# Optimization experiments

Hardware: AMD Instinct MI355X
Metric: run time of the kernel (lower is better)

The kernel has to match this reference:

```python
import jax, jax.numpy as jnp
import numpy as np

B, S, F_IN, D, H, L, E, DFF, OUT = 16, 512, 46, 256, 8, 6, 8, 1024, 3


def _ln(x, s, b, eps=1e-5):
    m = x.mean(-1, keepdims=True)
    v = ((x - m) ** 2).mean(-1, keepdims=True)
    return (x - m) / jnp.sqrt(v + eps) * s + b


def _mha(q_in, kv_in, qkv_w, qkv_b, out_w, out_b, h):
    # torch nn.MultiheadAttention (batch_first), eval mode (no dropout)
    d = q_in.shape[-1]
    dh = d // h
    wq, wk, wv = jnp.split(qkv_w, 3, axis=0)
    bq, bk, bv = jnp.split(qkv_b, 3)
    q = (q_in @ wq.T + bq).reshape(q_in.shape[0], q_in.shape[1], h, dh)
    k = (kv_in @ wk.T + bk).reshape(kv_in.shape[0], kv_in.shape[1], h, dh)
    v = (kv_in @ wv.T + bv).reshape(kv_in.shape[0], kv_in.shape[1], h, dh)
    attn = jax.nn.softmax(jnp.einsum('bqhd,bkhd->bhqk', q, k) / jnp.sqrt(jnp.float32(dh)), axis=-1)
    o = jnp.einsum('bhqk,bkhd->bqhd', attn, v).reshape(q_in.shape[0], q_in.shape[1], d)
    return o @ out_w.T + out_b


def _moe(x, gate_w, gate_b, e_w1, e_b1, e_w2, e_b2, top_k=2):
    # Faithful to source: EVERY expert runs its dense FFN over all tokens,
    # then outputs are mixed by the top-k gate weights (zero for unrouted experts).
    logits = x @ gate_w.T + gate_b                      # (B,S,E)
    tk_logits, tk_idx = jax.lax.top_k(logits, top_k)    # (B,S,K)
    tk_probs = jax.nn.softmax(tk_logits, axis=-1)
    onehot = jax.nn.one_hot(tk_idx, logits.shape[-1], dtype=x.dtype)  # (B,S,K,E)
    weights = (onehot * tk_probs[..., None]).sum(-2)    # (B,S,E)
    hid = jax.nn.gelu(jnp.einsum('bsd,efd->bsef', x, e_w1) + e_b1, approximate=False)  # (B,S,E,DFF)
    out_e = jnp.einsum('bsef,edf->bsed', hid, e_w2) + e_b2                             # (B,S,E,D)
    out = jnp.einsum('bsed,bse->bsd', out_e, weights)
    probs = jax.nn.softmax(logits, axis=-1)
    aux = logits.shape[-1] * jnp.sum(probs.mean(axis=(0, 1)) ** 2)
    return out, aux


def _posenc(s, d):
    pos = jnp.arange(s, dtype=jnp.float32)[:, None]
    div = jnp.exp(jnp.arange(0, d, 2, dtype=jnp.float32) * (-np.log(10000.0) / d))
    pe = jnp.zeros((s, d), jnp.float32)
    pe = pe.at[:, 0::2].set(jnp.sin(pos * div)).at[:, 1::2].set(jnp.cos(pos * div))
    return pe


def _forward(x, in_w, in_b, l_qkv_w, l_qkv_b, l_out_w, l_out_b, gate_w, gate_b,
             e_w1, e_b1, e_w2, e_b2, ln1_s, ln1_b, ln2_s, ln2_b,
             p_qkv_w, p_qkv_b, p_out_w, p_out_b,
             a_w1, a_b1, a_ln1s, a_ln1b, a_w2, a_b2, a_ln2s, a_ln2b, a_w3, a_b3,
             pr_w1, pr_b1, pr_ln1s, pr_ln1b, pr_w2, pr_b2, pr_ln2s, pr_ln2b, pr_w3, pr_b3):
    h = x @ in_w.T + in_b + _posenc(x.shape[1], D)[None]
    aux_total = jnp.float32(0.0)
    # NB: source builds ModuleList([encoder_layer]*L) with the SAME instance -> shared weights
    for _ in range(L):
        attn = _mha(h, h, l_qkv_w, l_qkv_b, l_out_w, l_out_b, H)
        h = _ln(h + attn, ln1_s, ln1_b)
        moe_out, aux = _moe(h, gate_w, gate_b, e_w1, e_b1, e_w2, e_b2)
        aux_total = aux_total + aux
        h = _ln(h + moe_out, ln2_s, ln2_b)
    pooled = _mha(h[:, -1:, :], h, p_qkv_w, p_qkv_b, p_out_w, p_out_b, H)[:, 0]  # (B,D)
    # action head: Linear -> GELU -> LN -> Linear -> GELU -> LN -> Linear
    a = jax.nn.gelu(pooled @ a_w1.T + a_b1, approximate=False)
    a = _ln(a, a_ln1s, a_ln1b)
    a = jax.nn.gelu(a @ a_w2.T + a_b2, approximate=False)
    a = _ln(a, a_ln2s, a_ln2b)
    action = a @ a_w3.T + a_b3
    # profit head: Linear -> LN -> GELU -> Linear -> LN -> GELU -> Linear
    p = jax.nn.gelu(_ln(pooled @ pr_w1.T + pr_b1, pr_ln1s, pr_ln1b), approximate=False)
    p = jax.nn.gelu(_ln(p @ pr_w2.T + pr_b2, pr_ln2s, pr_ln2b), approximate=False)
    profit = p @ pr_w3.T + pr_b3
    return action, profit, aux_total


def setup_inputs() -> dict:
    key = jax.random.key(0)
    ks = iter(jax.random.split(key, 64))
    def w(shape, scale=0.02):
        return jax.random.normal(next(ks), shape, jnp.float32) * scale
    d2, d4 = D // 2, D // 4
    return dict(
        x=jax.random.normal(next(ks), (B, S, F_IN), jnp.float32),
        in_w=w((D, F_IN)), in_b=jnp.zeros(D),
        l_qkv_w=w((3 * D, D)), l_qkv_b=jnp.zeros(3 * D), l_out_w=w((D, D)), l_out_b=jnp.zeros(D),
        gate_w=w((E, D)), gate_b=jnp.zeros(E),
        e_w1=w((E, DFF, D)), e_b1=jnp.zeros((E, DFF)), e_w2=w((E, D, DFF)), e_b2=jnp.zeros((E, D)),
        ln1_s=jnp.ones(D), ln1_b=jnp.zeros(D), ln2_s=jnp.ones(D), ln2_b=jnp.zeros(D),
        p_qkv_w=w((3 * D, D)), p_qkv_b=jnp.zeros(3 * D), p_out_w=w((D, D)), p_out_b=jnp.zeros(D),
        a_w1=w((d2, D)), a_b1=jnp.zeros(d2), a_ln1s=jnp.ones(d2), a_ln1b=jnp.zeros(d2),
        a_w2=w((d4, d2)), a_b2=jnp.zeros(d4), a_ln2s=jnp.ones(d4), a_ln2b=jnp.zeros(d4),
        a_w3=w((OUT, d4)), a_b3=jnp.zeros(OUT),
        pr_w1=w((D, D)), pr_b1=jnp.zeros(D), pr_ln1s=jnp.ones(D), pr_ln1b=jnp.zeros(D),
        pr_w2=w((d2, D)), pr_b2=jnp.zeros(d2), pr_ln2s=jnp.ones(d2), pr_ln2b=jnp.zeros(d2),
        pr_w3=w((1, d2)), pr_b3=jnp.zeros(1),
    )


def reference(x, in_w, in_b, l_qkv_w, l_qkv_b, l_out_w, l_out_b, gate_w, gate_b,
              e_w1, e_b1, e_w2, e_b2, ln1_s, ln1_b, ln2_s, ln2_b,
              p_qkv_w, p_qkv_b, p_out_w, p_out_b,
              a_w1, a_b1, a_ln1s, a_ln1b, a_w2, a_b2, a_ln2s, a_ln2b, a_w3, a_b3,
              pr_w1, pr_b1, pr_ln1s, pr_ln1b, pr_w2, pr_b2, pr_ln2s, pr_ln2b, pr_w3, pr_b3):
    return _forward(x, in_w, in_b, l_qkv_w, l_qkv_b, l_out_w, l_out_b, gate_w, gate_b,
                    e_w1, e_b1, e_w2, e_b2, ln1_s, ln1_b, ln2_s, ln2_b,
                    p_qkv_w, p_qkv_b, p_out_w, p_out_b,
                    a_w1, a_b1, a_ln1s, a_ln1b, a_w2, a_b2, a_ln2s, a_ln2b, a_w3, a_b3,
                    pr_w1, pr_b1, pr_ln1s, pr_ln1b, pr_w2, pr_b2, pr_ln2s, pr_ln2b, pr_w3, pr_b3)
```

## Files before the change

### kernel.cpp

```cpp
#include <hip/hip_runtime.h>
#include <hip/hip_bf16.h>
#include <math.h>


typedef __bf16 bf16;
typedef __bf16 bf16x8 __attribute__((ext_vector_type(8)));
typedef __bf16 bf16x4 __attribute__((ext_vector_type(4)));
typedef float f32x4 __attribute__((ext_vector_type(4)));

#define NIN 41

#define GLOAD_LDS(g, l)                                                    \
    __builtin_amdgcn_global_load_lds(                                      \
        (const __attribute__((address_space(1))) void*)(g),                \
        (__attribute__((address_space(3))) void*)(l), 16, 0, 0)

struct InTab {
    const void* src[NIN];
    unsigned off[NIN];
    unsigned n[NIN];
};

__device__ __forceinline__ float gelu_exact(float x) {
    return 0.5f * x * (1.0f + erff(x * 0.70710678118654752f));
// ... 125 lines not shown
            }
#pragma unroll
            for (int mt = 0; mt < MT; mt++)
#pragma unroll
                for (int nt = 0; nt < NT; nt++)
                    acc[mt][nt] = __builtin_amdgcn_mfma_f32_16x16x32_bf16(
                        af[mt], bfr[nt], acc[mt][nt], 0, 0, 0);
        }
        __syncthreads();
    }

    if (VTOUT && bn0g >= 512) {
#pragma unroll
        for (int mt = 0; mt < MT; mt++)
#pragma unroll
            for (int nt = 0; nt < NT; nt++) {
                const int gn = bn0g + wn0 + nt * 16 + frow;
                const float bv = (float)bias[gn];
                bf16x4 o4;
#pragma unroll
                for (int r = 0; r < 4; r++) o4[r] = (bf16)(acc[mt][nt][r] + bv);
                const int gm0 = bm0 + wm0 + mt * 16 + fquad * 4;
                const int d = gn - 512;
                *(bf16x4*)&vT[((size_t)((gm0 >> 9) * 8 + (d >> 5)) * 32 + (d & 31)) * 512 +
                              (gm0 & 511)] = o4;
            }
    } else {
        bf16* Cs = smem;
#pragma unroll
        for (int mt = 0; mt < MT; mt++)
#pragma unroll
            for (int nt = 0; nt < NT; nt++) {
                const int cl = wn0 + nt * 16 + frow;
                const float bv = (float)bias[bn0g + cl];
#pragma unroll
                for (int r = 0; r < 4; r++)
                    Cs[(wm0 + mt * 16 + fquad * 4 + r) * BN + cl] =
                        (bf16)(acc[mt][nt][r] + bv);
            }
        __syncthreads();
        constexpr int CPR = BN / 8;
        constexpr int CH = (BM * BN) / (256 * 8);
#pragma unroll
        for (int i = 0; i < CH; i++) {
            const int ch = tid + i * 256;
            const int row = ch / CPR;
            const int col = (ch % CPR) * 8;
            *(bf16x8*)&C[(size_t)(bm0 + row) * N + bn0g + col] =
                *(const bf16x8*)&Cs[row * BN + col];
        }
    }
}

__global__ __launch_bounds__(256) void gemm_moe_w1(
    const bf16* __restrict__ A, const bf16* __restrict__ Wb,
    const bf16* __restrict__ biasb, bf16* __restrict__ hid0,
    bf16* __restrict__ hid1, const int* __restrict__ list,
    const int* __restrict__ tile_ex, const int* __restrict__ ntiles) {
    constexpr int BM = 64, BN = 128, BK = 64;
    constexpr int N = 1024, K = 256;
    const int slot = (blockIdx.x >= 144) ? 1 : 0;
    const int xi = (int)blockIdx.x - slot * 144;
    if (xi >= (ntiles[slot] << 1)) return;
    __shared__ alignas(16) bf16 smem[BM * BK + BN * BK];
    bf16* As = smem;
    bf16* Ws = smem + BM * BK;
    const int* mylist = list + slot * 9216;
    const int e = tile_ex[slot * 72 + (xi >> 1)];
    const bf16* W = Wb + (size_t)e * N * K;
    const bf16* bias = biasb + e * N;
    bf16* C = slot ? hid1 : hid0;
    const int bm0 = xi * BM, bn0 = blockIdx.y * BN;
    const int tid = threadIdx.x;
    const int wave = tid >> 6, lane = tid & 63;
    const int wm0 = (wave >> 1) * 32, wn0 = (wave & 1) * 64;
    constexpr int MT = 2, NT = 4;
    f32x4 acc[MT][NT] = {};
    const int frow = lane & 15, fquad = lane >> 4;

    const bf16* ag[2];
    const bf16* bg[4];
    unsigned al[2], bl[4];
#pragma unroll
    for (int i = 0; i < 2; i++) {
        const int d = wave * 128 + i * 64 + lane;
        const int r = d >> 3, c = ((d & 7) ^ (r & 7)) * 8;
        ag[i] = A + (size_t)mylist[bm0 + r] * K + c;
        al[i] = (unsigned)(wave * 128 + i * 64) * 8u;
    }
#pragma unroll
    for (int i = 0; i < 4; i++) {
        const int d = wave * 256 + i * 64 + lane;
        const int r = d >> 3, c = ((d & 7) ^ (r & 7)) * 8;
        bg[i] = W + (size_t)(bn0 + r) * K + c;
        bl[i] = (unsigned)(wave * 256 + i * 64) * 8u;
    }

    for (int k0 = 0; k0 < K; k0 += BK) {
#pragma unroll
        for (int i = 0; i < 2; i++) GLOAD_LDS(ag[i] + k0, &As[al[i]]);
#pragma unroll
        for (int i = 0; i < 4; i++) GLOAD_LDS(bg[i] + k0, &Ws[bl[i]]);
        __syncthreads();
#pragma unroll
        for (int ks = 0; ks < 2; ks++) {
            bf16x8 af[MT], bfr[NT];
#pragma unroll
            for (int mt = 0; mt < MT; mt++) {
                const int r = wm0 + mt * 16 + frow;
                af[mt] = *(const bf16x8*)&As[SWZ(r, ks * 4 + fquad)];
            }
#pragma unroll
            for (int nt = 0; nt < NT; nt++) {
                const int r = wn0 + nt * 16 + frow;
                bfr[nt] = *(const bf16x8*)&Ws[SWZ(r, ks * 4 + fquad)];
            }
#pragma unroll
            for (int mt = 0; mt < MT; mt++)
#pragma unroll
                for (int nt = 0; nt < NT; nt++)
                    acc[mt][nt] = __builtin_amdgcn_mfma_f32_16x16x32_bf16(
                        af[mt], bfr[nt], acc[mt][nt], 0, 0, 0);
        }
        __syncthreads();
    }

    {
        bf16* Cs = smem;
#pragma unroll
        for (int mt = 0; mt < MT; mt++)
#pragma unroll
            for (int nt = 0; nt < NT; nt++) {
                const int cl = wn0 + nt * 16 + frow;
                const float bv = (float)bias[bn0 + cl];
#pragma unroll
                for (int r = 0; r < 4; r++)
                    Cs[(wm0 + mt * 16 + fquad * 4 + r) * BN + cl] =
                        (bf16)gelu_fast(acc[mt][nt][r] + bv);
            }
        __syncthreads();
#pragma unroll
        for (int i = 0; i < 4; i++) {
            const int ch = tid + i * 256;
            const int row = ch >> 4;
            const int col = (ch & 15) * 8;
            *(bf16x8*)&C[(size_t)(bm0 + row) * N + bn0 + col] =
                *(const bf16x8*)&Cs[row * BN + col];
        }
    }
}

__global__ __launch_bounds__(256) void gemm_moe_w2(
    const bf16* __restrict__ hid0, const bf16* __restrict__ hid1,
    const bf16* __restrict__ Wb, const bf16* __restrict__ biasb,
    bf16* __restrict__ moe0, bf16* __restrict__ moe1,
    const int* __restrict__ list, const float* __restrict__ lw,
    const int* __restrict__ tile_ex, const int* __restrict__ ntiles) {
    constexpr int BM = 64, BN = 64, BK = 64;
    constexpr int N = 256, K = 1024;
    const int slot = (blockIdx.x >= 144) ? 1 : 0;
    const int xi = (int)blockIdx.x - slot * 144;
    if (xi >= (ntiles[slot] << 1)) return;
    __shared__ alignas(16) bf16 smem[BM * BK + BN * BK];
    bf16* As = smem;
    bf16* Ws = smem + BM * BK;
    const bf16* A = slot ? hid1 : hid0;
    bf16* C = slot ? moe1 : moe0;
    const int* mylist = list + slot * 9216;
    const float* mylw = lw + slot * 9216;
    const int e = tile_ex[slot * 72 + (xi >> 1)];
    const bf16* W = Wb + (size_t)e * N * K;
    const bf16* bias = biasb + e * N;
    const int bm0 = xi * BM, bn0 = blockIdx.y * BN;
    const int tid = threadIdx.x;
    const int wave = tid >> 6, lane = tid & 63;
    const int wm0 = wave * 16;
    constexpr int NT = 4;
    f32x4 acc[NT] = {};
    const int frow = lane & 15, fquad = lane >> 4;

    const bf16* ag[2];
    const bf16* bg[2];
    unsigned al[2], bl[2];
#pragma unroll
    for (int i = 0; i < 2; i++) {
        const int d = wave * 128 + i * 64 + lane;
        const int r = d >> 3, c = ((d & 7) ^ (r & 7)) * 8;
        ag[i] = A + (size_t)(bm0 + r) * K + c;
        al[i] = (unsigned)(wave * 128 + i * 64) * 8u;
        bg[i] = W + (size_t)(bn0 + r) * K + c;
        bl[i] = al[i];
    }

    for (int k0 = 0; k0 < K; k0 += BK) {
#pragma unroll
        for (int i = 0; i < 2; i++) GLOAD_LDS(ag[i] + k0, &As[al[i]]);
#pragma unroll
        for (int i = 0; i < 2; i++) GLOAD_LDS(bg[i] + k0, &Ws[bl[i]]);
        __syncthreads();
#pragma unroll
        for (int ks = 0; ks < 2; ks++) {
            bf16x8 af, bfr[NT];
            af = *(const bf16x8*)&As[SWZ(wm0 + frow, ks * 4 + fquad)];
#pragma unroll
            for (int nt = 0; nt < NT; nt++) {
                const int r = nt * 16 + frow;
                bfr[nt] = *(const bf16x8*)&Ws[SWZ(r, ks * 4 + fquad)];
            }
#pragma unroll
            for (int nt = 0; nt < NT; nt++)
                acc[nt] = __builtin_amdgcn_mfma_f32_16x16x32_bf16(
                    af, bfr[nt], acc[nt], 0, 0, 0);
        }
        __syncthreads();
    }

    {
        bf16* Cs = smem;
        float lwv[4];
#pragma unroll
        for (int r = 0; r < 4; r++)
            lwv[r] = mylw[bm0 + wm0 + fquad * 4 + r];
#pragma unroll
        for (int nt = 0; nt < NT; nt++) {
            const int cl = nt * 16 + frow;
            const float bv = (float)bias[bn0 + cl];
#pragma unroll
            for (int r = 0; r < 4; r++)
                Cs[(wm0 + fquad * 4 + r) * BN + cl] =
                    (bf16)(lwv[r] * (acc[nt][r] + bv));
        }
        __syncthreads();
#pragma unroll
        for (int i = 0; i < 2; i++) {
            const int ch = tid + i * 256;
            const int row = ch >> 3;
            const int col = (ch & 7) * 8;
            *(bf16x8*)&C[(size_t)mylist[bm0 + row] * 256 + bn0 + col] =
                *(const bf16x8*)&Cs[row * BN + col];
        }
    }
}

__global__ __launch_bounds__(256) void input_proj_kernel(
    const bf16* __restrict__ x, const bf16* __restrict__ w,
    const bf16* __restrict__ b, bf16* __restrict__ h) {
    const int m = blockIdx.x, t = threadIdx.x;
    __shared__ float xs[46];
    if (t < 46) xs[t] = (float)x[m * 46 + t];
    __syncthreads();
    float acc = (float)b[t];
#pragma unroll
    for (int k = 0; k < 46; k++) acc += xs[k] * (float)w[t * 46 + k];
    const int s = m & 511;
    const int i = t >> 1;
    const float dv = expf((float)(2 * i) * (-9.210340371976184f / 256.0f));
    const float ang = (float)s * dv;
    const float pe = (t & 1) ? cosf(ang) : sinf(ang);
    h[(size_t)m * 256 + t] = (bf16)(acc + pe);
}

__global__ __launch_bounds__(256) void ln_kernel(
    bf16* __restrict__ h, const bf16* __restrict__ a0,
    const bf16* __restrict__ a1, const bf16* __restrict__ s,
    const bf16* __restrict__ b) {
    const int wv = threadIdx.x >> 6, lane = threadIdx.x & 63;
    const int m = blockIdx.x * 8 + wv * 2 + (lane >> 5);
    const int c0 = (lane & 31) * 8;
    const size_t off = (size_t)m * 256 + c0;
    bf16x8 hv = *(const bf16x8*)&h[off];
    bf16x8 av = *(const bf16x8*)&a0[off];
    bf16x8 bv2 = *(const bf16x8*)&a1[off];
    float x[8];
    float s1 = 0.0f, s2 = 0.0f;
#pragma unroll
    for (int j = 0; j < 8; j++) {
        x[j] = (float)hv[j] + (float)av[j] + (float)bv2[j];
        s1 += x[j];
        s2 += x[j] * x[j];
    }
#pragma unroll
    for (int msk = 1; msk < 32; msk <<= 1) {
        s1 += __shfl_xor(s1, msk, 64);
        s2 += __shfl_xor(s2, msk, 64);
    }
    const float mean = s1 * (1.0f / 256.0f);
    const float var = fmaxf(s2 * (1.0f / 256.0f) - mean * mean, 0.0f);
    const float inv = rsqrtf(var + 1e-5f);
    bf16x8 sv = *(const bf16x8*)&s[c0];
    bf16x8 bv = *(const bf16x8*)&b[c0];
    bf16x8 o;
#pragma unroll
    for (int j = 0; j < 8; j++)
        o[j] = (bf16)((x[j] - mean) * inv * (float)sv[j] + (float)bv[j]);
    *(bf16x8*)&h[off] = o;
}

__global__ __launch_bounds__(256) void proj_gate_ln_kernel(
    const bf16* __restrict__ A, const bf16* __restrict__ W,
    const bf16* __restrict__ bias, bf16* __restrict__ h,
    const bf16* __restrict__ lns, const bf16* __restrict__ lnb,
    const bf16* __restrict__ gw, const bf16* __restrict__ gb,
    int* __restrict__ top_e, float* __restrict__ top_w,
    int* __restrict__ g_hist, float* __restrict__ aux_sums) {
    __shared__ alignas(16) bf16 As[16 * 64];
    __shared__ alignas(16) bf16 Ws[256 * 64];
    __shared__ alignas(16) bf16 hs[16 * 264];
    __shared__ alignas(16) bf16 gws[8 * 264];
    __shared__ float rws1[4][16], rws2[4][16];
    __shared__ float meanv[16], invv[16];
    __shared__ float lg[128];
    __shared__ int sh_hist[16];
    __shared__ float sh_aux[8];

    const int bm0 = blockIdx.x * 16;
    const int tid = threadIdx.x;
    const int wave = tid >> 6, lane = tid & 63;
    const int wn0 = wave * 64;
    const int frow = lane & 15, fquad = lane >> 4;
    f32x4 acc[4] = {};

    const int da = (wave & 1) * 64 + lane;
    const int ra = da >> 3, ca = ((da & 7) ^ (ra & 7)) * 8;
    const bf16* ag = A + (size_t)(bm0 + ra) * 256 + ca;
    const unsigned al = (unsigned)((wave & 1) * 64) * 8u;
    const bf16* bg[8];
    unsigned bl[8];
#pragma unroll
    for (int i = 0; i < 8; i++) {
        const int d = wave * 512 + i * 64 + lane;
        const int r = d >> 3, c = ((d & 7) ^ (r & 7)) * 8;
        bg[i] = W + (size_t)r * 256 + c;
        bl[i] = (unsigned)(wave * 512 + i * 64) * 8u;
    }

    {
        const int rr = tid >> 4, ccb = (tid & 15) * 16;
        const bf16* src = &h[(size_t)(bm0 + rr) * 256 + ccb];
        bf16x8 v0 = *(const bf16x8*)&src[0];
        bf16x8 v1 = *(const bf16x8*)&src[8];
        bf16* dst = &hs[rr * 264 + ccb];
        *(bf16x8*)&dst[0] = v0;
        *(bf16x8*)&dst[8] = v1;
    }
    {
        const int e = tid >> 5, k = (tid & 31) * 8;
        *(bf16x8*)&gws[e * 264 + k] = *(const bf16x8*)&gw[e * 256 + k];
    }
    if (tid < 16) sh_hist[tid] = 0;
    if (tid < 8) sh_aux[tid] = 0.0f;

    for (int k0 = 0; k0 < 256; k0 += 64) {
        if (wave < 2) GLOAD_LDS(ag + k0, &As[al]);
#pragma unroll
        for (int i = 0; i < 8; i++) GLOAD_LDS(bg[i] + k0, &Ws[bl[i]]);
        __syncthreads();
#pragma unroll
        for (int ks = 0; ks < 2; ks++) {
            bf16x8 af, bfr[4];
            af = *(const bf16x8*)&As[SWZ(frow, ks * 4 + fquad)];
#pragma unroll
            for (int nt = 0; nt < 4; nt++)
                bfr[nt] = *(const bf16x8*)&Ws[SWZ(wn0 + nt * 16 + frow, ks * 4 + fquad)];
#pragma unroll
            for (int nt = 0; nt < 4; nt++)
                acc[nt] = __builtin_amdgcn_mfma_f32_16x16x32_bf16(
                    af, bfr[nt], acc[nt], 0, 0, 0);
        }
        __syncthreads();
    }

    float s1v[4] = {}, s2v[4] = {};
#pragma unroll
    for (int nt = 0; nt < 4; nt++) {
        const int gn = wn0 + nt * 16 + frow;
        const float bv = (float)bias[gn];
#pragma unroll
        for (int r = 0; r < 4; r++) {
            const int row = fquad * 4 + r;
            const float x = acc[nt][r] + bv + (float)hs[row * 264 + gn];
            acc[nt][r] = x;
            s1v[r] += x;
            s2v[r] += x * x;
        }
    }
#pragma unroll
    for (int r = 0; r < 4; r++) {
#pragma unroll
        for (int m = 1; m < 16; m <<= 1) {
            s1v[r] += __shfl_xor(s1v[r], m, 64);
            s2v[r] += __shfl_xor(s2v[r], m, 64);
        }
    }
    if (frow == 0) {
#pragma unroll
        for (int r = 0; r < 4; r++) {
            const int row = fquad * 4 + r;
            rws1[wave][row] = s1v[r];
            rws2[wave][row] = s2v[r];
        }
    }
    __syncthreads();
    if (tid < 16) {
        const float a = rws1[0][tid] + rws1[1][tid] + rws1[2][tid] + rws1[3][tid];
        const float c2 = rws2[0][tid] + rws2[1][tid] + rws2[2][tid] + rws2[3][tid];
        const float mean = a * (1.0f / 256.0f);
        const float var = fmaxf(c2 * (1.0f / 256.0f) - mean * mean, 0.0f);
        meanv[tid] = mean;
        invv[tid] = rsqrtf(var + 1e-5f);
    }
    __syncthreads();

#pragma unroll
    for (int nt = 0; nt < 4; nt++) {
        const int gn = wn0 + nt * 16 + frow;
        const float sg = (float)lns[gn], bgn = (float)lnb[gn];
#pragma unroll
        for (int r = 0; r < 4; r++) {
            const int row = fquad * 4 + r;
            const float o = (acc[nt][r] - meanv[row]) * invv[row] * sg + bgn;
            hs[row * 264 + gn] = (bf16)o;
        }
    }
    __syncthreads();

    {
        const int rr = tid >> 4, ccb = (tid & 15) * 16;
        bf16* dst = &h[(size_t)(bm0 + rr) * 256 + ccb];
        const bf16* src = &hs[rr * 264 + ccb];
        *(bf16x8*)&dst[0] = *(const bf16x8*)&src[0];
        *(bf16x8*)&dst[8] = *(const bf16x8*)&src[8];
    }
    if (tid < 128) {
        const int row = tid >> 3, e = tid & 7;
        float acg = (float)gb[e];
        for (int k = 0; k < 256; k += 8) {
            bf16x8 hv = *(const bf16x8*)&hs[row * 264 + k];
            bf16x8 wv = *(const bf16x8*)&gws[e * 264 + k];
#pragma unroll
            for (int q = 0; q < 8; q++) acg += (float)hv[q] * (float)wv[q];
        }
        lg[row * 8 + e] = acg;
    }
    __syncthreads();

    if (tid < 16) {
        const int tok = bm0 + tid;
        float l[8];
#pragma unroll
        for (int j = 0; j < 8; j++) l[j] = lg[tid * 8 + j];
        int i0 = 0;
#pragma unroll
        for (int j = 1; j < 8; j++)
            if (l[j] > l[i0]) i0 = j;
        int i1 = -1;
#pragma unroll
        for (int j = 0; j < 8; j++)
            if (j != i0 && (i1 < 0 || l[j] > l[i1])) i1 = j;
        const float p0 = 1.0f / (1.0f + expf(l[i1] - l[i0]));
        top_e[tok] = i0;         top_w[tok] = p0;
        top_e[8192 + tok] = i1;  top_w[8192 + tok] = 1.0f - p0;
        atomicAdd(&sh_hist[i0], 1);
        atomicAdd(&sh_hist[8 + i1], 1);
        const float mx = l[i0];
        float se = 0.0f;
#pragma unroll
        for (int j = 0; j < 8; j++) { l[j] = expf(l[j] - mx); se += l[j]; }
        const float si = 1.0f / se;
#pragma unroll
        for (int j = 0; j < 8; j++) atomicAdd(&sh_aux[j], l[j] * si);
    }
    __syncthreads();
    if (tid < 16) g_hist[blockIdx.x * 16 + tid] = sh_hist[tid];
    if (tid < 8) atomicAdd(&aux_sums[tid], sh_aux[tid]);
}

__global__ __launch_bounds__(256) void scatter_route_kernel(
    const int* __restrict__ g_hist, const int* __restrict__ top_e,
    const float* __restrict__ top_w, int* __restrict__ ntiles,
    int* __restrict__ tile_ex, int* __restrict__ list, float* __restrict__ lw) {
    __shared__ int gh[512][16];
    __shared__ int ps[16][8];
    __shared__ int s_cnt[16], s_pre[16], s_off[16], pos[16];
    const int tid = threadIdx.x;
    for (int i = tid; i < 8192; i += 256) gh[i >> 4][i & 15] = g_hist[i];
    __syncthreads();
    if (tid < 128) {
        const int se = tid >> 3, ch = tid & 7;
        int s = 0;
        for (int b = ch * 64; b < ch * 64 + 64; b++) s += gh[b][se];
        ps[se][ch] = s;
    }
    __syncthreads();
    if (tid < 16) {
        int run = 0;
        for (int ch = 0; ch < 8; ch++) run += ps[tid][ch];
        const int b0 = (int)blockIdx.x * 8;
        int pre = 0;
        for (int ch = 0; ch < (b0 >> 6); ch++) pre += ps[tid][ch];
        for (int b = b0 & ~63; b < b0; b++) pre += gh[b][tid];
        s_cnt[tid] = run;
        s_pre[tid] = pre;
    }
    __syncthreads();
    if (tid < 2) {
        const int slot = tid;
        int o = 0;
        for (int e2 = 0; e2 < 8; e2++) {
            s_off[slot * 8 + e2] = o;
            const int nt = (s_cnt[slot * 8 + e2] + 127) >> 7;
            if (blockIdx.x == 0)
                for (int t = 0; t < nt; t++) tile_ex[slot * 72 + (o >> 7) + t] = e2;
            o += nt << 7;
        }
        if (blockIdx.x == 0) ntiles[slot] = o >> 7;
    }
    __syncthreads();
    if (tid < 16) pos[tid] = s_off[tid] + s_pre[tid];
    __syncthreads();
    if (blockIdx.x == 0) {
        for (int idx = tid; idx < 16 * 128; idx += 256) {
            const int seg = idx >> 7, i = idx & 127;
            const int slot = seg >> 3;
            const int start = s_off[seg] + s_cnt[seg];
            const int end = s_off[seg] + ((s_cnt[seg] + 127) & ~127);
            const int p = start + i;
            if (p < end) {
                list[slot * 9216 + p] = 8192;
                lw[slot * 9216 + p] = 0.0f;
            }
        }
    }
    if (tid < 128) {
        const int tok = blockIdx.x * 128 + tid;
#pragma unroll
        for (int slot = 0; slot < 2; slot++) {
            const int e = top_e[slot * 8192 + tok];
            const float w = top_w[slot * 8192 + tok];
            const int idx = atomicAdd(&pos[slot * 8 + e], 1);
            list[slot * 9216 + idx] = tok;
            lw[slot * 9216 + idx] = w;
        }
    }
}

__global__ __launch_bounds__(256) void attn_kernel(
    const bf16* __restrict__ qkv, const bf16* __restrict__ vT,
    bf16* __restrict__ aout) {
    __shared__ alignas(16) bf16 P[32][520];
    __shared__ float wsum[4][32];
    __shared__ float sinv[32];
    const int s0 = blockIdx.x * 32;
    const int b = blockIdx.y >> 3, hh = blockIdx.y & 7;
    const int tid = threadIdx.x, wave = tid >> 6, lane = tid & 63;
    const int frow = lane & 15, fquad = lane >> 4;
    const size_t base = (size_t)b * 512;
    const float CST = 0.25505654f;

    bf16x8 qf[2];
#pragma unroll
    for (int mt = 0; mt < 2; mt++)
        qf[mt] = *(const bf16x8*)&qkv[(base + s0 + mt * 16 + frow) * 768 + hh * 32 + fquad * 8];
    float rsum[2][4] = {};
#pragma unroll
    for (int k8 = 0; k8 < 8; k8++) {
        const int key0 = (wave * 8 + k8) * 16;
        bf16x8 kf = *(const bf16x8*)&qkv[(base + key0 + frow) * 768 + 256 + hh * 32 + fquad * 8];
#pragma unroll
        for (int mt = 0; mt < 2; mt++) {
            f32x4 c = {};
            c = __builtin_amdgcn_mfma_f32_16x16x32_bf16(qf[mt], kf, c, 0, 0, 0);
#pragma unroll
            for (int r = 0; r < 4; r++) {
                const float e_ = __builtin_exp2f(fminf(c[r] * CST, 60.0f));
                P[mt * 16 + fquad * 4 + r][key0 + frow] = (bf16)e_;
                rsum[mt][r] += e_;
            }
        }
    }
#pragma unroll
    for (int mt = 0; mt < 2; mt++)
#pragma unroll
        for (int r = 0; r < 4; r++) {
#pragma unroll
            for (int m = 1; m < 16; m <<= 1)
                rsum[mt][r] += __shfl_xor(rsum[mt][r], m, 64);
        }
    if (frow == 0) {
#pragma unroll
        for (int mt = 0; mt < 2; mt++)
#pragma unroll
            for (int r = 0; r < 4; r++)
                wsum[wave][mt * 16 + fquad * 4 + r] = rsum[mt][r];
    }
    __syncthreads();
    if (tid < 32)
// ... 233 lines not shown
        for (int m = 1; m < 64; m <<= 1) {
            s1 += __shfl_xor(s1, m, 64);
            s2 += __shfl_xor(s2, m, 64);
        }
        if (lane == 0) { red[wave * 2] = s1; red[wave * 2 + 1] = s2; }
    }
    __syncthreads();
    if (t < 64) {
        const float S1 = red[0], S2 = red[1];
        const float mean = S1 * (1.0f / 64.0f);
        const float var = fmaxf(S2 * (1.0f / 64.0f) - mean * mean, 0.0f);
        const float inv = rsqrtf(var + 1e-5f);
        buf2a[t] = (buf2a[t] - mean) * inv * (float)aln2s[t] + (float)aln2b[t];
    } else if (t >= 128) {
        const int u = t - 128;
        const float S1 = red[4] + red[6], S2 = red[5] + red[7];
        const float mean = S1 * (1.0f / 128.0f);
        const float var = fmaxf(S2 * (1.0f / 128.0f) - mean * mean, 0.0f);
        const float inv = rsqrtf(var + 1e-5f);
        buf2p[u] = gelu_exact((buf2p[u] - mean) * inv *
                              (float)pln2s[u] + (float)pln2b[u]);
    }
    __syncthreads();

    if (t < 3) {
        float a = (float)ab3[t];
        for (int k = 0; k < 64; k++) a += buf2a[k] * (float)aw3[t * 64 + k];
        out[b * 3 + t] = a;
    }
    {
        float p = 0.0f;
        if (t >= 128) p = buf2p[t - 128] * (float)pw3[t - 128];
#pragma unroll
        for (int m = 1; m < 64; m <<= 1) p += __shfl_xor(p, m, 64);
        if (lane == 0) red[wave] = p;
    }
    __syncthreads();
    if (t == 0) out[48 + b] = (float)pb3[0] + red[2] + red[3];
}

extern "C" void kernel_launch(void* const* d_in, const int* in_sizes, int n_in,
                              void* d_out, int out_size, void* d_ws, size_t ws_size,
                              hipStream_t stream) {
    char* ws = (char*)d_ws;
    const size_t MB = 1024 * 1024;
    bf16*  h     = (bf16*)(ws);
    bf16*  moe0  = (bf16*)(ws + 8 * MB);
    bf16*  moe1  = (bf16*)(ws + 13 * MB);
    char*  ctrl  = ws + 20 * MB;
    float* auxs   = (float*)(ctrl + 0);
    int*   flag   = (int*)(ctrl + 192);
    int*   ntiles = (int*)(ctrl + 256);
    int*   tileex = (int*)(ctrl + 320);
    float* ostage = (float*)(ctrl + 1024);
    int*   g_hist = (int*)(ctrl + 2048);
    int*   top_e  = (int*)(ctrl + 36864);
    float* top_w  = (float*)(ctrl + 102400);
    int*   list   = (int*)(ctrl + 167936);
    float* lw     = (float*)(ctrl + 241664);
    bf16*  qkv   = (bf16*)(ws + 24 * MB);
    bf16*  aoutb = (bf16*)(ws + 40 * MB);
    bf16*  hid0  = (bf16*)(ws + 56 * MB);
    bf16*  hid1  = (bf16*)(ws + 80 * MB);
    bf16*  vT    = (bf16*)(ws + 104 * MB);
    float* pattn = (float*)(ws + 110 * MB);
    bf16*  cvbase = (bf16*)(ws + 112 * MB);

    InTab tab;
    unsigned off = 0;
    bf16* cv[NIN];
    for (int i = 0; i < NIN; i++) {
        tab.src[i] = d_in[i];
        tab.off[i] = off;
        tab.n[i] = (unsigned)in_sizes[i];
        cv[i] = cvbase + off;
        off += ((unsigned)in_sizes[i] + 1023u) & ~1023u;
    }
    const int cv_blocks = (int)(off >> 10);

    const bf16 *x = cv[0], *in_w = cv[1], *in_b = cv[2], *qkv_w = cv[3], *qkv_b = cv[4],
               *out_w = cv[5], *out_b = cv[6], *gate_w = cv[7], *gate_b = cv[8],
               *e_w1 = cv[9], *e_b1 = cv[10], *e_w2 = cv[11], *e_b2 = cv[12],
               *ln1_s = cv[13], *ln1_b = cv[14], *ln2_s = cv[15], *ln2_b = cv[16],
               *pqkv_w = cv[17], *pqkv_b = cv[18], *pout_w = cv[19], *pout_b = cv[20],
               *a_w1 = cv[21], *a_b1 = cv[22], *a_ln1s = cv[23], *a_ln1b = cv[24],
               *a_w2 = cv[25], *a_b2 = cv[26], *a_ln2s = cv[27], *a_ln2b = cv[28],
               *a_w3 = cv[29], *a_b3 = cv[30],
               *pr_w1 = cv[31], *pr_b1 = cv[32], *pr_ln1s = cv[33], *pr_ln1b = cv[34],
               *pr_w2 = cv[35], *pr_b2 = cv[36], *pr_ln2s = cv[37], *pr_ln2b = cv[38],
               *pr_w3 = cv[39], *pr_b3 = cv[40];

    sniff_kernel<<<1, 256, 0, stream>>>((const unsigned*)d_in[0], flag);
    convert_kernel<<<cv_blocks, 256, 0, stream>>>(tab, cvbase, flag);

    hipMemsetAsync(auxs, 0, 192, stream);
    hipMemsetAsync((char*)h + (size_t)8192 * 512, 0, 512, stream);
    input_proj_kernel<<<8192, 256, 0, stream>>>(x, in_w, in_b, h);

    for (int l = 0; l < 6; l++) {
        gemm_bt<64, 128, 32, 64, true><<<dim3(128, 6), 256, 0, stream>>>(
            h, qkv_w, qkv_b, qkv, 8192, 768, 256, vT, 0);
        attn_kernel<<<dim3(16, 128), 256, 0, stream>>>(qkv, vT, aoutb);
        proj_gate_ln_kernel<<<512, 256, 0, stream>>>(
            aoutb, out_w, out_b, h, ln1_s, ln1_b, gate_w, gate_b,
            top_e, top_w, g_hist, auxs + l * 8);
        scatter_route_kernel<<<64, 256, 0, stream>>>(g_hist, top_e, top_w,
                                                     ntiles, tileex, list, lw);
        gemm_moe_w1<<<dim3(288, 8), 256, 0, stream>>>(
            h, e_w1, e_b1, hid0, hid1, list, tileex, ntiles);
        gemm_moe_w2<<<dim3(288, 4), 256, 0, stream>>>(
            hid0, hid1, e_w2, e_b2, moe0, moe1, list, lw, tileex, ntiles);
        ln_kernel<<<1024, 256, 0, stream>>>(h, moe0, moe1, ln2_s, ln2_b);
    }

    gemm_bt<64, 128, 32, 64, true><<<dim3(128, 4), 256, 0, stream>>>(
        h, pqkv_w, pqkv_b, qkv, 8192, 768, 256, vT, 256);
    pooled_attn_kernel<<<128, 256, 0, stream>>>(qkv, vT, h, pqkv_w, pqkv_b, pattn);
    heads_kernel<<<16, 256, 0, stream>>>(
        pattn, pout_w, pout_b,
        a_w1, a_b1, a_ln1s, a_ln1b, a_w2, a_b2, a_ln2s, a_ln2b, a_w3, a_b3,
        pr_w1, pr_b1, pr_ln1s, pr_ln1b, pr_w2, pr_b2, pr_ln2s, pr_ln2b, pr_w3, pr_b3,
        ostage);
    out_convert_kernel<<<1, 128, 0, stream>>>(ostage, auxs, d_out, flag);
}
```

Before: 949.0 us.

## Fuse MoE token scatter into gate kernel via global atomics and finer tiles

The gate kernel now claims per-expert slots with global atomic counters and writes token indices and weights straight into fixed-capacity per-expert lists. This replaces the separate multi-block histogram/prefix-scan scatter kernel with a tiny single-block kernel that only builds the tile table and pads each segment. Tile granularity drops from 128 to 64 rows, with an explicit per-tile base offset, to cut padding waste in the expert GEMMs. The price is global atomics in the gate kernel, a nondeterministic token order within each expert, and a counter reset placed in the following LN kernel.

```diff
diff --git a/kernel.cpp b/kernel.cpp
--- a/kernel.cpp
+++ b/kernel.cpp
@@ -201,21 +201,58 @@
     }
 }
 
+__global__ __launch_bounds__(256) void route_build_kernel(
+    const int* __restrict__ gcnt, int* __restrict__ ntiles,
+    int* __restrict__ tile_ex, int* __restrict__ tile_base,
+    int* __restrict__ list, float* __restrict__ lw) {
+    __shared__ int cnt[16];
+    const int t = threadIdx.x;
+    if (t < 16) cnt[t] = gcnt[t];
+    __syncthreads();
+    if (t < 2) {
+        const int slot = t;
+        int T = 0;
+        for (int e = 0; e < 8; e++) {
+            const int c = cnt[slot * 8 + e];
+            const int nt = (c + 63) >> 6;
+            for (int k = 0; k < nt; k++) {
+                tile_ex[slot * 160 + T] = e;
+                tile_base[slot * 160 + T] = e * 8192 + k * 64;
+                T++;
+            }
+        }
+        ntiles[slot] = T;
+    }
+    for (int i = t; i < 1024; i += 256) {
+        const int seg = i >> 6, j = i & 63;
+        const int c = cnt[seg];
+        const int rc = (c + 63) & ~63;
+        const int p = c + j;
+        if (p < rc) {
+            const int slot = seg >> 3, e = seg & 7;
+            list[slot * 65536 + e * 8192 + p] = 8192;
+            lw[slot * 65536 + e * 8192 + p] = 0.0f;
+        }
+    }
+}
+
 __global__ __launch_bounds__(256) void gemm_moe_w1(
     const bf16* __restrict__ A, const bf16* __restrict__ Wb,
     const bf16* __restrict__ biasb, bf16* __restrict__ hid0,
     bf16* __restrict__ hid1, const int* __restrict__ list,
-    const int* __restrict__ tile_ex, const int* __restrict__ ntiles) {
+    const int* __restrict__ tile_ex, const int* __restrict__ tile_base,
+    const int* __restrict__ ntiles) {
     constexpr int BM = 64, BN = 128, BK = 64;
     constexpr int N = 1024, K = 256;
     const int slot = (blockIdx.x >= 144) ? 1 : 0;
     const int xi = (int)blockIdx.x - slot * 144;
-    if (xi >= (ntiles[slot] << 1)) return;
+    if (xi >= ntiles[slot]) return;
     __shared__ alignas(16) bf16 smem[BM * BK + BN * BK];
     bf16* As = smem;
     bf16* Ws = smem + BM * BK;
-    const int* mylist = list + slot * 9216;
-    const int e = tile_ex[slot * 72 + (xi >> 1)];
+    const int* mylist = list + slot * 65536;
+    const int e = tile_ex[slot * 160 + xi];
+    const int tb = tile_base[slot * 160 + xi];
     const bf16* W = Wb + (size_t)e * N * K;
     const bf16* bias = biasb + e * N;
     bf16* C = slot ? hid1 : hid0;
@@ -234,7 +271,7 @@
     for (int i = 0; i < 2; i++) {
         const int d = wave * 128 + i * 64 + lane;
         const int r = d >> 3, c = ((d & 7) ^ (r & 7)) * 8;
-        ag[i] = A + (size_t)mylist[bm0 + r] * K + c;
+        ag[i] = A + (size_t)mylist[tb + r] * K + c;
         al[i] = (unsigned)(wave * 128 + i * 64) * 8u;
     }
 #pragma unroll
@@ -304,20 +341,22 @@
     const bf16* __restrict__ Wb, const bf16* __restrict__ biasb,
     bf16* __restrict__ moe0, bf16* __restrict__ moe1,
     const int* __restrict__ list, const float* __restrict__ lw,
-    const int* __restrict__ tile_ex, const int* __restrict__ ntiles) {
+    const int* __restrict__ tile_ex, const int* __restrict__ tile_base,
+    const int* __restrict__ ntiles) {
     constexpr int BM = 64, BN = 64, BK = 64;
     constexpr int N = 256, K = 1024;
     const int slot = (blockIdx.x >= 144) ? 1 : 0;
     const int xi = (int)blockIdx.x - slot * 144;
-    if (xi >= (ntiles[slot] << 1)) return;
+    if (xi >= ntiles[slot]) return;
     __shared__ alignas(16) bf16 smem[BM * BK + BN * BK];
     bf16* As = smem;
     bf16* Ws = smem + BM * BK;
     const bf16* A = slot ? hid1 : hid0;
     bf16* C = slot ? moe1 : moe0;
-    const int* mylist = list + slot * 9216;
-    const float* mylw = lw + slot * 9216;
-    const int e = tile_ex[slot * 72 + (xi >> 1)];
+    const int* mylist = list + slot * 65536;
+    const float* mylw = lw + slot * 65536;
+    const int e = tile_ex[slot * 160 + xi];
+    const int tb = tile_base[slot * 160 + xi];
     const bf16* W = Wb + (size_t)e * N * K;
     const bf16* bias = biasb + e * N;
     const int bm0 = xi * BM, bn0 = blockIdx.y * BN;
@@ -369,7 +408,7 @@
         float lwv[4];
 #pragma unroll
         for (int r = 0; r < 4; r++)
-            lwv[r] = mylw[bm0 + wm0 + fquad * 4 + r];
+            lwv[r] = mylw[tb + wm0 + fquad * 4 + r];
 #pragma unroll
         for (int nt = 0; nt < NT; nt++) {
             const int cl = nt * 16 + frow;
@@ -385,7 +424,7 @@
             const int ch = tid + i * 256;
             const int row = ch >> 3;
             const int col = (ch & 7) * 8;
-            *(bf16x8*)&C[(size_t)mylist[bm0 + row] * 256 + bn0 + col] =
+            *(bf16x8*)&C[(size_t)mylist[tb + row] * 256 + bn0 + col] =
                 *(const bf16x8*)&Cs[row * BN + col];
         }
     }
@@ -412,7 +451,8 @@
 __global__ __launch_bounds__(256) void ln_kernel(
     bf16* __restrict__ h, const bf16* __restrict__ a0,
     const bf16* __restrict__ a1, const bf16* __restrict__ s,
-    const bf16* __restrict__ b) {
+    const bf16* __restrict__ b, int* __restrict__ gcnt) {
+    if (blockIdx.x == 0 && threadIdx.x < 16) gcnt[threadIdx.x] = 0;
     const int wv = threadIdx.x >> 6, lane = threadIdx.x & 63;
     const int m = blockIdx.x * 8 + wv * 2 + (lane >> 5);
     const int c0 = (lane & 31) * 8;
@@ -450,8 +490,8 @@
     const bf16* __restrict__ bias, bf16* __restrict__ h,
     const bf16* __restrict__ lns, const bf16* __restrict__ lnb,
     const bf16* __restrict__ gw, const bf16* __restrict__ gb,
-    int* __restrict__ top_e, float* __restrict__ top_w,
-    int* __restrict__ g_hist, float* __restrict__ aux_sums) {
+    int* __restrict__ gcnt, int* __restrict__ list, float* __restrict__ lw,
+    float* __restrict__ aux_sums) {
     __shared__ alignas(16) bf16 As[16 * 64];
     __shared__ alignas(16) bf16 Ws[256 * 64];
     __shared__ alignas(16) bf16 hs[16 * 264];
@@ -460,6 +500,9 @@
     __shared__ float meanv[16], invv[16];
     __shared__ float lg[128];
     __shared__ int sh_hist[16];
+    __shared__ int sel0[16], sel1[16];
+    __shared__ float wt0[16], wt1[16];
+    __shared__ int sh_base[16];
     __shared__ float sh_aux[8];
 
     const int bm0 = blockIdx.x * 16;
@@ -594,7 +637,6 @@
     __syncthreads();
 
     if (tid < 16) {
-        const int tok = bm0 + tid;
         float l[8];
 #pragma unroll
         for (int j = 0; j < 8; j++) l[j] = lg[tid * 8 + j];
@@ -607,8 +649,8 @@
         for (int j = 0; j < 8; j++)
             if (j != i0 && (i1 < 0 || l[j] > l[i1])) i1 = j;
         const float p0 = 1.0f / (1.0f + expf(l[i1] - l[i0]));
-        top_e[tok] = i0;         top_w[tok] = p0;
-        top_e[8192 + tok] = i1;  top_w[8192 + tok] = 1.0f - p0;
+        sel0[tid] = i0;  wt0[tid] = p0;
+        sel1[tid] = i1;  wt1[tid] = 1.0f - p0;
         atomicAdd(&sh_hist[i0], 1);
         atomicAdd(&sh_hist[8 + i1], 1);
         const float mx = l[i0];
@@ -620,77 +662,25 @@
         for (int j = 0; j < 8; j++) atomicAdd(&sh_aux[j], l[j] * si);
     }
     __syncthreads();
-    if (tid < 16) g_hist[blockIdx.x * 16 + tid] = sh_hist[tid];
+    if (tid < 16 && sh_hist[tid] > 0)
+        sh_base[tid] = atomicAdd(&gcnt[tid], sh_hist[tid]);
+    __syncthreads();
+    if (tid < 16) {
+        const int tok = bm0 + tid;
+        const int e0 = sel0[tid], e1 = sel1[tid];
+        int off0 = 0, off1 = 0;
+        for (int j = 0; j < tid; j++) {
+            if (sel0[j] == e0) off0++;
+            if (sel1[j] == e1) off1++;
+        }
+        const int p0 = sh_base[e0] + off0;
+        const int p1 = sh_base[8 + e1] + off1;
+        list[e0 * 8192 + p0] = tok;
+        lw[e0 * 8192 + p0] = wt0[tid];
+        list[65536 + e1 * 8192 + p1] = tok;
+        lw[65536 + e1 * 8192 + p1] = wt1[tid];
+    }
     if (tid < 8) atomicAdd(&aux_sums[tid], sh_aux[tid]);
-}
-
-__global__ __launch_bounds__(256) void scatter_route_kernel(
-    const int* __restrict__ g_hist, const int* __restrict__ top_e,
-    const float* __restrict__ top_w, int* __restrict__ ntiles,
-    int* __restrict__ tile_ex, int* __restrict__ list, float* __restrict__ lw) {
-    __shared__ int gh[512][16];
-    __shared__ int ps[16][8];
-    __shared__ int s_cnt[16], s_pre[16], s_off[16], pos[16];
-    const int tid = threadIdx.x;
-    for (int i = tid; i < 8192; i += 256) gh[i >> 4][i & 15] = g_hist[i];
-    __syncthreads();
-    if (tid < 128) {
-        const int se = tid >> 3, ch = tid & 7;
-        int s = 0;
-        for (int b = ch * 64; b < ch * 64 + 64; b++) s += gh[b][se];
-        ps[se][ch] = s;
-    }
-    __syncthreads();
-    if (tid < 16) {
-        int run = 0;
-        for (int ch = 0; ch < 8; ch++) run += ps[tid][ch];
-        const int b0 = (int)blockIdx.x * 8;
-        int pre = 0;
-        for (int ch = 0; ch < (b0 >> 6); ch++) pre += ps[tid][ch];
-        for (int b = b0 & ~63; b < b0; b++) pre += gh[b][tid];
-        s_cnt[tid] = run;
-        s_pre[tid] = pre;
-    }
-    __syncthreads();
-    if (tid < 2) {
-        const int slot = tid;
-        int o = 0;
-        for (int e2 = 0; e2 < 8; e2++) {
-            s_off[slot * 8 + e2] = o;
-            const int nt = (s_cnt[slot * 8 + e2] + 127) >> 7;
-            if (blockIdx.x == 0)
-                for (int t = 0; t < nt; t++) tile_ex[slot * 72 + (o >> 7) + t] = e2;
-            o += nt << 7;
-        }
-        if (blockIdx.x == 0) ntiles[slot] = o >> 7;
-    }
-    __syncthreads();
-    if (tid < 16) pos[tid] = s_off[tid] + s_pre[tid];
-    __syncthreads();
-    if (blockIdx.x == 0) {
-        for (int idx = tid; idx < 16 * 128; idx += 256) {
-            const int seg = idx >> 7, i = idx & 127;
-            const int slot = seg >> 3;
-            const int start = s_off[seg] + s_cnt[seg];
-            const int end = s_off[seg] + ((s_cnt[seg] + 127) & ~127);
-            const int p = start + i;
-            if (p < end) {
-                list[slot * 9216 + p] = 8192;
-                lw[slot * 9216 + p] = 0.0f;
-            }
-        }
-    }
-    if (tid < 128) {
-        const int tok = blockIdx.x * 128 + tid;
-#pragma unroll
-        for (int slot = 0; slot < 2; slot++) {
-            const int e = top_e[slot * 8192 + tok];
-            const float w = top_w[slot * 8192 + tok];
-            const int idx = atomicAdd(&pos[slot * 8 + e], 1);
-            list[slot * 9216 + idx] = tok;
-            lw[slot * 9216 + idx] = w;
-        }
-    }
 }
 
 __global__ __launch_bounds__(256) void attn_kernel(
@@ -1030,12 +1020,11 @@
     int*   flag   = (int*)(ctrl + 192);
     int*   ntiles = (int*)(ctrl + 256);
     int*   tileex = (int*)(ctrl + 320);
-    float* ostage = (float*)(ctrl + 1024);
-    int*   g_hist = (int*)(ctrl + 2048);
-    int*   top_e  = (int*)(ctrl + 36864);
-    float* top_w  = (float*)(ctrl + 102400);
-    int*   list   = (int*)(ctrl + 167936);
-    float* lw     = (float*)(ctrl + 241664);
+    int*   tilebs = (int*)(ctrl + 1664);
+    float* ostage = (float*)(ctrl + 3072);
+    int*   gcnt   = (int*)(ctrl + 3584);
+    int*   list   = (int*)(ctrl + 4096);
+    float* lw     = (float*)(ctrl + 4096 + 524288);
     bf16*  qkv   = (bf16*)(ws + 24 * MB);
     bf16*  aoutb = (bf16*)(ws + 40 * MB);
     bf16*  hid0  = (bf16*)(ws + 56 * MB);
@@ -1072,6 +1061,7 @@
     convert_kernel<<<cv_blocks, 256, 0, stream>>>(tab, cvbase, flag);
 
     hipMemsetAsync(auxs, 0, 192, stream);
+    hipMemsetAsync(gcnt, 0, 64, stream);
     hipMemsetAsync((char*)h + (size_t)8192 * 512, 0, 512, stream);
     input_proj_kernel<<<8192, 256, 0, stream>>>(x, in_w, in_b, h);
 
@@ -1081,14 +1071,14 @@
         attn_kernel<<<dim3(16, 128), 256, 0, stream>>>(qkv, vT, aoutb);
         proj_gate_ln_kernel<<<512, 256, 0, stream>>>(
             aoutb, out_w, out_b, h, ln1_s, ln1_b, gate_w, gate_b,
-            top_e, top_w, g_hist, auxs + l * 8);
-        scatter_route_kernel<<<64, 256, 0, stream>>>(g_hist, top_e, top_w,
-                                                     ntiles, tileex, list, lw);
+            gcnt, list, lw, auxs + l * 8);
+        route_build_kernel<<<1, 256, 0, stream>>>(
+            gcnt, ntiles, tileex, tilebs, list, lw);
         gemm_moe_w1<<<dim3(288, 8), 256, 0, stream>>>(
-            h, e_w1, e_b1, hid0, hid1, list, tileex, ntiles);
+            h, e_w1, e_b1, hid0, hid1, list, tileex, tilebs, ntiles);
         gemm_moe_w2<<<dim3(288, 4), 256, 0, stream>>>(
-            hid0, hid1, e_w2, e_b2, moe0, moe1, list, lw, tileex, ntiles);
-        ln_kernel<<<1024, 256, 0, stream>>>(h, moe0, moe1, ln2_s, ln2_b);
+            hid0, hid1, e_w2, e_b2, moe0, moe1, list, lw, tileex, tilebs, ntiles);
+        ln_kernel<<<1024, 256, 0, stream>>>(h, moe0, moe1, ln2_s, ln2_b, gcnt);
     }
 
     gemm_bt<64, 128, 32, 64, true><<<dim3(128, 4), 256, 0, stream>>>(
```

Measured after the change: 977.2 us. +3.0%, slower.

## Split fused out-projection+LN+gate kernel into separate GEMM and LN/gate kernels

Applied to the files above, without the earlier changes.

Replaces the fused out-projection/residual/LayerNorm/gate kernel with a generic tiled GEMM writing to a temporary buffer, followed by a lightweight LN+gate kernel that reads the projection and residual. The intent is to get better occupancy and parallelism for the projection GEMM (more, smaller tiles than the 512-block fused kernel with its large shared-memory W tile). In exchange it adds an extra kernel launch and a global round trip of the projection output, and the bias is now applied in bf16 before the residual add, which changes rounding.

```diff
diff --git a/kernel.cpp b/kernel.cpp
--- a/kernel.cpp
+++ b/kernel.cpp
@@ -445,53 +445,22 @@
     *(bf16x8*)&h[off] = o;
 }
 
-__global__ __launch_bounds__(256) void proj_gate_ln_kernel(
-    const bf16* __restrict__ A, const bf16* __restrict__ W,
-    const bf16* __restrict__ bias, bf16* __restrict__ h,
+__global__ __launch_bounds__(256) void ln_gate_kernel(
+    const bf16* __restrict__ proj, bf16* __restrict__ h,
     const bf16* __restrict__ lns, const bf16* __restrict__ lnb,
     const bf16* __restrict__ gw, const bf16* __restrict__ gb,
     int* __restrict__ top_e, float* __restrict__ top_w,
     int* __restrict__ g_hist, float* __restrict__ aux_sums) {
-    __shared__ alignas(16) bf16 As[16 * 64];
-    __shared__ alignas(16) bf16 Ws[256 * 64];
     __shared__ alignas(16) bf16 hs[16 * 264];
     __shared__ alignas(16) bf16 gws[8 * 264];
-    __shared__ float rws1[4][16], rws2[4][16];
-    __shared__ float meanv[16], invv[16];
     __shared__ float lg[128];
     __shared__ int sh_hist[16];
     __shared__ float sh_aux[8];
 
     const int bm0 = blockIdx.x * 16;
     const int tid = threadIdx.x;
-    const int wave = tid >> 6, lane = tid & 63;
-    const int wn0 = wave * 64;
-    const int frow = lane & 15, fquad = lane >> 4;
-    f32x4 acc[4] = {};
-
-    const int da = (wave & 1) * 64 + lane;
-    const int ra = da >> 3, ca = ((da & 7) ^ (ra & 7)) * 8;
-    const bf16* ag = A + (size_t)(bm0 + ra) * 256 + ca;
-    const unsigned al = (unsigned)((wave & 1) * 64) * 8u;
-    const bf16* bg[8];
-    unsigned bl[8];
-#pragma unroll
-    for (int i = 0; i < 8; i++) {
-        const int d = wave * 512 + i * 64 + lane;
-        const int r = d >> 3, c = ((d & 7) ^ (r & 7)) * 8;
-        bg[i] = W + (size_t)r * 256 + c;
-        bl[i] = (unsigned)(wave * 512 + i * 64) * 8u;
-    }
-
-    {
-        const int rr = tid >> 4, ccb = (tid & 15) * 16;
-        const bf16* src = &h[(size_t)(bm0 + rr) * 256 + ccb];
-        bf16x8 v0 = *(const bf16x8*)&src[0];
-        bf16x8 v1 = *(const bf16x8*)&src[8];
-        bf16* dst = &hs[rr * 264 + ccb];
-        *(bf16x8*)&dst[0] = v0;
-        *(bf16x8*)&dst[8] = v1;
-    }
+    const int row = tid >> 4, seg = tid & 15;
+
     {
         const int e = tid >> 5, k = (tid & 31) * 8;
         *(bf16x8*)&gws[e * 264 + k] = *(const bf16x8*)&gw[e * 256 + k];
@@ -499,97 +468,58 @@
     if (tid < 16) sh_hist[tid] = 0;
     if (tid < 8) sh_aux[tid] = 0.0f;
 
-    for (int k0 = 0; k0 < 256; k0 += 64) {
-        if (wave < 2) GLOAD_LDS(ag + k0, &As[al]);
-#pragma unroll
-        for (int i = 0; i < 8; i++) GLOAD_LDS(bg[i] + k0, &Ws[bl[i]]);
-        __syncthreads();
-#pragma unroll
-        for (int ks = 0; ks < 2; ks++) {
-            bf16x8 af, bfr[4];
-            af = *(const bf16x8*)&As[SWZ(frow, ks * 4 + fquad)];
-#pragma unroll
-            for (int nt = 0; nt < 4; nt++)
-                bfr[nt] = *(const bf16x8*)&Ws[SWZ(wn0 + nt * 16 + frow, ks * 4 + fquad)];
-#pragma unroll
-            for (int nt = 0; nt < 4; nt++)
-                acc[nt] = __builtin_amdgcn_mfma_f32_16x16x32_bf16(
-                    af, bfr[nt], acc[nt], 0, 0, 0);
-        }
-        __syncthreads();
-    }
-
-    float s1v[4] = {}, s2v[4] = {};
-#pragma unroll
-    for (int nt = 0; nt < 4; nt++) {
-        const int gn = wn0 + nt * 16 + frow;
-        const float bv = (float)bias[gn];
-#pragma unroll
-        for (int r = 0; r < 4; r++) {
-            const int row = fquad * 4 + r;
-            const float x = acc[nt][r] + bv + (float)hs[row * 264 + gn];
-            acc[nt][r] = x;
-            s1v[r] += x;
-            s2v[r] += x * x;
-        }
-    }
-#pragma unroll
-    for (int r = 0; r < 4; r++) {
-#pragma unroll
-        for (int m = 1; m < 16; m <<= 1) {
-            s1v[r] += __shfl_xor(s1v[r], m, 64);
-            s2v[r] += __shfl_xor(s2v[r], m, 64);
-        }
-    }
-    if (frow == 0) {
-#pragma unroll
-        for (int r = 0; r < 4; r++) {
-            const int row = fquad * 4 + r;
-            rws1[wave][row] = s1v[r];
-            rws2[wave][row] = s2v[r];
-        }
-    }
-    __syncthreads();
-    if (tid < 16) {
-        const float a = rws1[0][tid] + rws1[1][tid] + rws1[2][tid] + rws1[3][tid];
-        const float c2 = rws2[0][tid] + rws2[1][tid] + rws2[2][tid] + rws2[3][tid];
-        const float mean = a * (1.0f / 256.0f);
-        const float var = fmaxf(c2 * (1.0f / 256.0f) - mean * mean, 0.0f);
-        meanv[tid] = mean;
-        invv[tid] = rsqrtf(var + 1e-5f);
-    }
-    __syncthreads();
-
-#pragma unroll
-    for (int nt = 0; nt < 4; nt++) {
-        const int gn = wn0 + nt * 16 + frow;
-        const float sg = (float)lns[gn], bgn = (float)lnb[gn];
-#pragma unroll
-        for (int r = 0; r < 4; r++) {
-            const int row = fquad * 4 + r;
-            const float o = (acc[nt][r] - meanv[row]) * invv[row] * sg + bgn;
-            hs[row * 264 + gn] = (bf16)o;
-        }
-    }
-    __syncthreads();
+    const size_t base = (size_t)(bm0 + row) * 256 + seg * 16;
+    bf16x8 p0 = *(const bf16x8*)&proj[base];
+    bf16x8 p1 = *(const bf16x8*)&proj[base + 8];
+    bf16x8 h0 = *(const bf16x8*)&h[base];
+    bf16x8 h1 = *(const bf16x8*)&h[base + 8];
+    float x[16];
+    float s1 = 0.0f, s2 = 0.0f;
+#pragma unroll
+    for (int j = 0; j < 8; j++) {
+        x[j] = (float)p0[j] + (float)h0[j];
+        x[8 + j] = (float)p1[j] + (float)h1[j];
+        s1 += x[j] + x[8 + j];
+        s2 += x[j] * x[j] + x[8 + j] * x[8 + j];
+    }
+#pragma unroll
+    for (int m = 1; m < 16; m <<= 1) {
+        s1 += __shfl_xor(s1, m, 64);
+        s2 += __shfl_xor(s2, m, 64);
+    }
+    const float mean = s1 * (1.0f / 256.0f);
+    const float var = fmaxf(s2 * (1.0f / 256.0f) - mean * mean, 0.0f);
+    const float inv = rsqrtf(var + 1e-5f);
 
     {
-        const int rr = tid >> 4, ccb = (tid & 15) * 16;
-        bf16* dst = &h[(size_t)(bm0 + rr) * 256 + ccb];
-        const bf16* src = &hs[rr * 264 + ccb];
-        *(bf16x8*)&dst[0] = *(const bf16x8*)&src[0];
-        *(bf16x8*)&dst[8] = *(const bf16x8*)&src[8];
-    }
+        bf16x8 sv0 = *(const bf16x8*)&lns[seg * 16];
+        bf16x8 sv1 = *(const bf16x8*)&lns[seg * 16 + 8];
+        bf16x8 bv0 = *(const bf16x8*)&lnb[seg * 16];
+        bf16x8 bv1 = *(const bf16x8*)&lnb[seg * 16 + 8];
+        bf16x8 o0, o1;
+#pragma unroll
+        for (int j = 0; j < 8; j++) {
+            o0[j] = (bf16)((x[j] - mean) * inv * (float)sv0[j] + (float)bv0[j]);
+            o1[j] = (bf16)((x[8 + j] - mean) * inv * (float)sv1[j] + (float)bv1[j]);
+        }
+        *(bf16x8*)&h[base] = o0;
+        *(bf16x8*)&h[base + 8] = o1;
+        bf16* dst = &hs[row * 264 + seg * 16];
+        *(bf16x8*)&dst[0] = o0;
+        *(bf16x8*)&dst[8] = o1;
+    }
+    __syncthreads();
+
     if (tid < 128) {
-        const int row = tid >> 3, e = tid & 7;
+        const int r8 = tid >> 3, e = tid & 7;
         float acg = (float)gb[e];
         for (int k = 0; k < 256; k += 8) {
-            bf16x8 hv = *(const bf16x8*)&hs[row * 264 + k];
+            bf16x8 hv = *(const bf16x8*)&hs[r8 * 264 + k];
             bf16x8 wv = *(const bf16x8*)&gws[e * 264 + k];
 #pragma unroll
             for (int q = 0; q < 8; q++) acg += (float)hv[q] * (float)wv[q];
         }
-        lg[row * 8 + e] = acg;
+        lg[r8 * 8 + e] = acg;
     }
     __syncthreads();
 
@@ -606,9 +536,9 @@
 #pragma unroll
         for (int j = 0; j < 8; j++)
             if (j != i0 && (i1 < 0 || l[j] > l[i1])) i1 = j;
-        const float p0 = 1.0f / (1.0f + expf(l[i1] - l[i0]));
-        top_e[tok] = i0;         top_w[tok] = p0;
-        top_e[8192 + tok] = i1;  top_w[8192 + tok] = 1.0f - p0;
+        const float p0w = 1.0f / (1.0f + expf(l[i1] - l[i0]));
+        top_e[tok] = i0;         top_w[tok] = p0w;
+        top_e[8192 + tok] = i1;  top_w[8192 + tok] = 1.0f - p0w;
         atomicAdd(&sh_hist[i0], 1);
         atomicAdd(&sh_hist[8 + i1], 1);
         const float mx = l[i0];
@@ -1038,6 +968,7 @@
     float* lw     = (float*)(ctrl + 241664);
     bf16*  qkv   = (bf16*)(ws + 24 * MB);
     bf16*  aoutb = (bf16*)(ws + 40 * MB);
+    bf16*  projtmp = (bf16*)(ws + 46 * MB);
     bf16*  hid0  = (bf16*)(ws + 56 * MB);
     bf16*  hid1  = (bf16*)(ws + 80 * MB);
     bf16*  vT    = (bf16*)(ws + 104 * MB);
@@ -1079,8 +1010,10 @@
         gemm_bt<64, 128, 32, 64, true><<<dim3(128, 6), 256, 0, stream>>>(
             h, qkv_w, qkv_b, qkv, 8192, 768, 256, vT, 0);
         attn_kernel<<<dim3(16, 128), 256, 0, stream>>>(qkv, vT, aoutb);
-        proj_gate_ln_kernel<<<512, 256, 0, stream>>>(
-            aoutb, out_w, out_b, h, ln1_s, ln1_b, gate_w, gate_b,
+        gemm_bt<32, 64, 16, 32, false><<<dim3(256, 4), 256, 0, stream>>>(
+            aoutb, out_w, out_b, projtmp, 8192, 256, 256, nullptr, 0);
+        ln_gate_kernel<<<512, 256, 0, stream>>>(
+            projtmp, h, ln1_s, ln1_b, gate_w, gate_b,
             top_e, top_w, g_hist, auxs + l * 8);
         scatter_route_kernel<<<64, 256, 0, stream>>>(g_hist, top_e, top_w,
                                                      ntiles, tileex, list, lw);
```

After: 939.3 us. No clear change (-1.0%).
